# Optimization experiments

Measured on AMD Instinct MI355X. Metric: run time of the kernel, lower is better.

## Reference

```python
import jax, jax.numpy as jnp
import numpy as np

LN_EPS = 1e-6


def setup_inputs() -> dict:
    key = jax.random.key(0)
    ks = jax.random.split(key, 8)
    B, T, V, r, c, D = 1, 2048, 50257, 16, 16, 1024
    rc = r * c
    return {
        "input_ids": jax.random.randint(ks[0], (B, T), 0, V),
        "token_to_mu_w": jax.random.normal(ks[1], (rc, V), jnp.float32) * 0.02,  # nn.Linear(V, rc).weight
        "pos_embedding": jax.random.normal(ks[2], (1, T, r, c), jnp.float32) * 0.02,
        "w1": jax.random.normal(ks[3], (D, rc), jnp.float32) * 0.05,  # Linear(rc, D).weight
        "b1": jnp.zeros((D,), jnp.float32),
        "ln_w": jnp.ones((D,), jnp.float32),
        "ln_b": jnp.zeros((D,), jnp.float32),
        "w2": jax.random.normal(ks[4], (V, D), jnp.float32) * 0.02,  # Linear(D, V).weight
        "b2": jnp.zeros((V,), jnp.float32),
    }


def reference(input_ids, token_to_mu_w, pos_embedding, w1, b1, ln_w, ln_b, w2, b2):
    B, T = input_ids.shape
    r, c = pos_embedding.shape[2], pos_embedding.shape[3]
    # one_hot(input_ids) @ W^T is exactly a row-gather of W^T (single nonzero per row)
    MU = jnp.take(token_to_mu_w.T, input_ids, axis=0)          # [B, T, rc]
    MU = MU.reshape(B, T, r, c) + pos_embedding[:, :T]         # [B, T, r, c]
    # n_layers = 0: no transformer blocks; dropout is identity in eval
    x = MU.reshape(B, T, r * c)
    h = jax.nn.gelu(jnp.einsum('btk,dk->btd', x, w1) + b1, approximate=False)
    mean = jnp.mean(h, axis=-1, keepdims=True)
    var = jnp.mean(jnp.square(h - mean), axis=-1, keepdims=True)
    h = (h - mean) * jax.lax.rsqrt(var + LN_EPS) * ln_w + ln_b
    logits = jnp.einsum('btd,vd->btv', h, w2) + b2             # [B, T, V]
    return logits, MU
```

## Files before the change

### kernel.cpp

```cpp
#include <hip/hip_runtime.h>
#include <hip/hip_bf16.h>
#include <math.h>

#define T_LEN 2048
#define RC 256
#define DIM 1024
#define VOCAB 50257
#define NT 32
#define SLOT 8192

using short8  = __attribute__((ext_vector_type(8))) short;
using f32x4   = __attribute__((ext_vector_type(4))) float;

#define VMCNT(n) asm volatile("s_waitcnt vmcnt(" #n ")" ::: "memory")
#define SCHED_FENCE() __builtin_amdgcn_sched_barrier(0)

__device__ __forceinline__ unsigned short f2bf(float f) {
    unsigned int u = __float_as_uint(f);
    u += 0x7fffu + ((u >> 16) & 1u);
    return (unsigned short)(u >> 16);
}

__device__ __forceinline__ unsigned int cvt_pk_bf16(float a, float b) {
    unsigned int r;
    asm volatile("v_cvt_pk_bf16_f32 %0, %1, %2" : "=v"(r) : "v"(a), "v"(b));
    return r;
}

__device__ __forceinline__ void async_load16(void* lds, const void* g) {
    __builtin_amdgcn_global_load_lds(
        (const __attribute__((address_space(1))) void*)g,
        (__attribute__((address_space(3))) void*)lds,
        16, 0, 0);
}

__global__ __launch_bounds__(256) void mu_kernel(
    const int* __restrict__ ids, const float* __restrict__ tokw,
    const float* __restrict__ pos, float* __restrict__ mu) {
    int t = blockIdx.x, k = threadIdx.x;
    int id = ids[t];
    float v = tokw[(size_t)k * VOCAB + id] + pos[t * RC + k];
    mu[t * RC + k] = v;
}

__global__ __launch_bounds__(256) void gemm1_gelu_kernel(
    const float* __restrict__ mu, const float* __restrict__ w1,
    const float* __restrict__ b1, float* __restrict__ hpre) {
    __shared__ float xs[16][RC];
    const int tg = blockIdx.x, ng = blockIdx.y, tid = threadIdx.x;
    const int t0 = tg * 16;
    {
        const float4* src = (const float4*)(mu + (size_t)t0 * RC);
        float4* dst = (float4*)&xs[0][0];
        #pragma unroll
        for (int i = 0; i < 4; ++i) dst[tid + 256 * i] = src[tid + 256 * i];
    }
    __syncthreads();
    const int d = ng * 256 + tid;
    float acc[16];
    const float bias = b1[d];
    #pragma unroll
    for (int t = 0; t < 16; ++t) acc[t] = bias;
    const float4* w1r = (const float4*)(w1 + (size_t)d * RC);
    for (int k4 = 0; k4 < RC / 4; ++k4) {
        const float4 w = w1r[k4];
        #pragma unroll
        for (int t = 0; t < 16; ++t) {
            const float4 xv = *(const float4*)&xs[t][k4 * 4];
            acc[t] += w.x * xv.x + w.y * xv.y + w.z * xv.z + w.w * xv.w;
        }
    }
    #pragma unroll
    for (int t = 0; t < 16; ++t) {
        float x = acc[t];
        float g = 0.5f * x * (1.0f + erff(x * 0.70710678118654752f));
        hpre[(size_t)(t0 + t) * DIM + d] = g;
    }
}

__global__ __launch_bounds__(256) void ln_kernel(
    const float* __restrict__ hpre, const float* __restrict__ lnw,
    const float* __restrict__ lnb, unsigned short* __restrict__ h) {
    const int t = blockIdx.x, tid = threadIdx.x;
    const float4 v = ((const float4*)(hpre + (size_t)t * DIM))[tid];
    float s  = v.x + v.y + v.z + v.w;
    float ss = v.x * v.x + v.y * v.y + v.z * v.z + v.w * v.w;
    #pragma unroll
    for (int off = 32; off > 0; off >>= 1) {
        s  += __shfl_down(s, off, 64);
        ss += __shfl_down(ss, off, 64);
    }
    __shared__ float red[8];
    const int wid = tid >> 6, lane = tid & 63;
    if (lane == 0) { red[wid] = s; red[4 + wid] = ss; }
    __syncthreads();
    const float S  = red[0] + red[1] + red[2] + red[3];
    const float SS = red[4] + red[5] + red[6] + red[7];
    const float mean = S * (1.0f / DIM);
    const float var  = SS * (1.0f / DIM) - mean * mean;
    const float inv  = 1.0f / sqrtf(var + 1e-6f);
    const float4 wv = ((const float4*)lnw)[tid];
    const float4 bv = ((const float4*)lnb)[tid];
    ushort4 o;
    o.x = f2bf((v.x - mean) * inv * wv.x + bv.x);
    o.y = f2bf((v.y - mean) * inv * wv.y + bv.y);
    o.z = f2bf((v.z - mean) * inv * wv.z + bv.z);
    o.w = f2bf((v.w - mean) * inv * wv.w + bv.w);
    ((ushort4*)h)[(size_t)t * (DIM / 4) + tid] = o;
}

__global__ __launch_bounds__(256) void cvt_kernel(
    const float* __restrict__ src, unsigned int* __restrict__ dst, int n8) {
    int i = blockIdx.x * 256 + threadIdx.x;
    const int stride = gridDim.x * 256;
    for (; i < n8; i += stride) {
        const float4 a = ((const float4*)src)[2 * i];
        const float4 b = ((const float4*)src)[2 * i + 1];
        uint4 o;
        o.x = cvt_pk_bf16(a.x, a.y);
        o.y = cvt_pk_bf16(a.z, a.w);
        o.z = cvt_pk_bf16(b.x, b.y);
        o.w = cvt_pk_bf16(b.z, b.w);
        ((uint4*)dst)[i] = o;
    }
}

__device__ __forceinline__ void stage_A512(
    const unsigned short* __restrict__ A, unsigned short* dst,
    int m0, int kt, int tid, int gsrc) {
    #pragma unroll
    for (int p = 0; p < 2; ++p) {
        const int idx = p * 512 + tid;
        const int row = idx >> 2;
        async_load16(dst + (size_t)idx * 8,
                     A + (size_t)(m0 + row) * DIM + kt * 32 + gsrc * 8);
    }
}
__device__ __forceinline__ void stage_B512(
    const unsigned short* __restrict__ B, unsigned short* dst,
    int n0, int kt, int tid, int gsrc) {
    #pragma unroll
    for (int p = 0; p < 2; ++p) {
        const int idx = p * 512 + tid;
        int row = n0 + (idx >> 2); if (row > VOCAB - 1) row = VOCAB - 1;
        async_load16(dst + (size_t)idx * 8,
                     B + (size_t)row * DIM + kt * 32 + gsrc * 8);
    }
}

__global__ __launch_bounds__(512, 2) void gemm2_kernel(
    const unsigned short* __restrict__ A, const unsigned short* __restrict__ B,
    const float* __restrict__ b2, float* __restrict__ out) {
    __shared__ unsigned short As[3 * SLOT];
    __shared__ unsigned short Bs[3 * SLOT];

    const int tid  = threadIdx.x;
    const int cpx  = gridDim.x >> 3;
    const int wgid = (blockIdx.x & 7) * cpx + (blockIdx.x >> 3);
    const int m0   = (wgid & 7) << 8;
    const int n0   = (wgid >> 3) << 8;

    const int lane = tid & 63;
    const int lr   = lane & 15;
    const int lk   = lane >> 4;
    const int wid  = tid >> 6;
    const int wr   = wid >> 2;
    const int wc   = wid & 3;
    const int xr   = (lk ^ ((lr >> 1) & 3)) * 8;
    const int arow0 = wr * 128 + lr;
    const int brow0 = wc * 64 + lr;
    const int gsrc = (tid & 3) ^ ((tid >> 3) & 3);

    f32x4 acc[8][4];
    #pragma unroll
    for (int m = 0; m < 8; ++m)
        #pragma unroll
        for (int n = 0; n < 4; ++n) acc[m][n] = {0.f, 0.f, 0.f, 0.f};

    stage_A512(A, As, m0, 0, tid, gsrc);
    stage_B512(B, Bs, n0, 0, tid, gsrc);
    SCHED_FENCE();
    stage_A512(A, As + SLOT, m0, 1, tid, gsrc);
    stage_B512(B, Bs + SLOT, n0, 1, tid, gsrc);
    SCHED_FENCE();
    VMCNT(4);
    __builtin_amdgcn_s_barrier();

    int cur = 0, st2 = 2;
    #pragma unroll 1
    for (int t = 0; t < NT; ++t) {
        const unsigned short* As_t = As + cur * SLOT;
        const unsigned short* Bs_t = Bs + cur * SLOT;
        short8 af[4], af2[4], bf[4];

        #pragma unroll
        for (int m = 0; m < 4; ++m)
            af[m] = *(const short8*)(As_t + (arow0 + m * 16) * 32 + xr);
        #pragma unroll
        for (int n = 0; n < 4; ++n)
            bf[n] = *(const short8*)(Bs_t + (brow0 + n * 16) * 32 + xr);
        if (t + 2 < NT)
            stage_A512(A, As + st2 * SLOT, m0, t + 2, tid, gsrc);
        SCHED_FENCE();
        __builtin_amdgcn_s_barrier();
        __builtin_amdgcn_s_setprio(1);
        #pragma unroll
        for (int m = 0; m < 4; ++m)
            #pragma unroll
            for (int n = 0; n < 4; ++n)
                acc[m][n] = __builtin_amdgcn_mfma_f32_16x16x32_bf16(
                    af[m], bf[n], acc[m][n], 0, 0, 0);
        __builtin_amdgcn_s_setprio(0);
        SCHED_FENCE();
        __builtin_amdgcn_s_barrier();

        #pragma unroll
        for (int m = 0; m < 4; ++m)
            af2[m] = *(const short8*)(As_t + (arow0 + (m + 4) * 16) * 32 + xr);
        if (t + 2 < NT)
            stage_B512(B, Bs + st2 * SLOT, n0, t + 2, tid, gsrc);
        SCHED_FENCE();
        if (t < NT - 2) { VMCNT(4); } else { VMCNT(0); }
        __builtin_amdgcn_s_barrier();
        __builtin_amdgcn_s_setprio(1);
        #pragma unroll
        for (int m = 0; m < 4; ++m)
            #pragma unroll
            for (int n = 0; n < 4; ++n)
                acc[m + 4][n] = __builtin_amdgcn_mfma_f32_16x16x32_bf16(
                    af2[m], bf[n], acc[m + 4][n], 0, 0, 0);
        __builtin_amdgcn_s_setprio(0);
        SCHED_FENCE();
        __builtin_amdgcn_s_barrier();

        cur = (cur == 2) ? 0 : cur + 1;
        st2 = (st2 == 2) ? 0 : st2 + 1;
    }

    float bias[4]; int col[4]; bool ok[4];
    #pragma unroll
    for (int n = 0; n < 4; ++n) {
        col[n] = n0 + wc * 64 + n * 16 + lr;
        ok[n]  = col[n] < VOCAB;
        bias[n] = ok[n] ? b2[col[n]] : 0.f;
    }
    #pragma unroll
    for (int m = 0; m < 8; ++m) {
        const int row = m0 + wr * 128 + m * 16 + lk * 4;
        #pragma unroll
        for (int n = 0; n < 4; ++n) {
            if (ok[n]) {
                #pragma unroll
                for (int j = 0; j < 4; ++j)
                    out[(size_t)(row + j) * VOCAB + col[n]] = acc[m][n][j] + bias[n];
            }
        }
    }
}

extern "C" void kernel_launch(void* const* d_in, const int* in_sizes, int n_in,
                              void* d_out, int out_size, void* d_ws, size_t ws_size,
                              hipStream_t stream) {
    (void)in_sizes; (void)n_in; (void)out_size; (void)ws_size;
    const int*   ids  = (const int*)d_in[0];
    const float* tokw = (const float*)d_in[1];
    const float* pos  = (const float*)d_in[2];
    const float* w1   = (const float*)d_in[3];
    const float* b1   = (const float*)d_in[4];
    const float* lnw  = (const float*)d_in[5];
    const float* lnb  = (const float*)d_in[6];
    const float* w2   = (const float*)d_in[7];
    const float* b2   = (const float*)d_in[8];

    float* logits = (float*)d_out;
    float* mu_out = logits + (size_t)T_LEN * VOCAB;

    unsigned short* w2b = (unsigned short*)d_ws;
    unsigned short* hb  = (unsigned short*)((char*)d_ws + (size_t)VOCAB * DIM * 2);
    float* hpre = logits;

    mu_kernel<<<dim3(T_LEN), dim3(256), 0, stream>>>(ids, tokw, pos, mu_out);
    gemm1_gelu_kernel<<<dim3(T_LEN / 16, DIM / 256), dim3(256), 0, stream>>>(
        mu_out, w1, b1, hpre);
    ln_kernel<<<dim3(T_LEN), dim3(256), 0, stream>>>(hpre, lnw, lnb, hb);
    cvt_kernel<<<dim3(2048), dim3(256), 0, stream>>>(
        w2, (unsigned int*)w2b, (int)((size_t)VOCAB * DIM / 8));
    const int ntiles_n = (VOCAB + 255) / 256;
    gemm2_kernel<<<dim3(8 * ntiles_n), dim3(512), 0, stream>>>(hb, w2b, b2, logits);
}
```

Before: 464.2 us.

## Deepen gemm2 LDS pipeline to four stages with register-prefetched fragments

The output GEMM's shared-memory ring grows from three to four slots, so global loads are issued three K-tiles ahead instead of two. The loop is unrolled by two with ping-pong B-fragment registers. The next tile's A and B fragments are read from LDS before the second MFMA half of the current tile, and fine-grained lgkmcnt waits replace some of the barriers, cutting the barriers per tile from four to two. The aim is to hide LDS and global-load latency behind MFMA work, at the cost of more LDS and more live registers.

```diff
diff --git a/kernel.cpp b/kernel.cpp
--- a/kernel.cpp
+++ b/kernel.cpp
@@ -13,6 +13,7 @@
 using f32x4   = __attribute__((ext_vector_type(4))) float;
 
 #define VMCNT(n) asm volatile("s_waitcnt vmcnt(" #n ")" ::: "memory")
+#define LGKM(n)  asm volatile("s_waitcnt lgkmcnt(" #n ")" ::: "memory")
 #define SCHED_FENCE() __builtin_amdgcn_sched_barrier(0)
 
 __device__ __forceinline__ unsigned short f2bf(float f) {
@@ -148,11 +149,66 @@
     }
 }
 
+#define TILE_BODY(T, BF_USE, BF_LOAD)                                          \
+  {                                                                            \
+    const int t_  = (T);                                                       \
+    const int cur = t_ & 3;                                                    \
+    const int nxt = (t_ + 1) & 3;                                              \
+    const int st  = (t_ + 3) & 3;                                              \
+    const unsigned short* As_t = As + cur * SLOT;                              \
+                       \
+    _Pragma("unroll")                                                          \
+    for (int m = 0; m < 4; ++m)                                                \
+        af_o[m] = *(const short8*)(As_t + (arow0 + (m + 4) * 16) * 32 + xr);   \
+    if (t_ + 3 < NT)                                                           \
+        stage_A512(A, As + st * SLOT, m0, t_ + 3, tid, gsrc);                  \
+    SCHED_FENCE();                                                             \
+    LGKM(4);                           \
+    SCHED_FENCE();                                                             \
+    __builtin_amdgcn_s_setprio(1);                                             \
+    _Pragma("unroll")                                                          \
+    for (int m = 0; m < 4; ++m)                                                \
+        _Pragma("unroll")                                                      \
+        for (int n = 0; n < 4; ++n)                                            \
+            acc[m][n] = __builtin_amdgcn_mfma_f32_16x16x32_bf16(               \
+                af_e[m], BF_USE[n], acc[m][n], 0, 0, 0);                       \
+    __builtin_amdgcn_s_setprio(0);                                             \
+    SCHED_FENCE();                                                             \
+    if (t_ + 3 < NT) { VMCNT(6); } else { VMCNT(0); }                          \
+    __builtin_amdgcn_s_barrier();        \
+                        \
+    if (t_ + 1 < NT) {                                                         \
+        const unsigned short* As_n = As + nxt * SLOT;                          \
+        const unsigned short* Bs_n = Bs + nxt * SLOT;                          \
+        _Pragma("unroll")                                                      \
+        for (int m = 0; m < 4; ++m)                                            \
+            af_e[m] = *(const short8*)(As_n + (arow0 + m * 16) * 32 + xr);     \
+        _Pragma("unroll")                                                      \
+        for (int n = 0; n < 4; ++n)                                            \
+            BF_LOAD[n] = *(const short8*)(Bs_n + (brow0 + n * 16) * 32 + xr);  \
+    }                                                                          \
+    if (t_ + 3 < NT)                                                           \
+        stage_B512(B, Bs + st * SLOT, n0, t_ + 3, tid, gsrc);                  \
+    SCHED_FENCE();                                                             \
+    if (t_ + 1 < NT) { LGKM(8); } else { LGKM(0); }           \
+    SCHED_FENCE();                                                             \
+    __builtin_amdgcn_s_setprio(1);                                             \
+    _Pragma("unroll")                                                          \
+    for (int m = 0; m < 4; ++m)                                                \
+        _Pragma("unroll")                                                      \
+        for (int n = 0; n < 4; ++n)                                            \
+            acc[m + 4][n] = __builtin_amdgcn_mfma_f32_16x16x32_bf16(           \
+                af_o[m], BF_USE[n], acc[m + 4][n], 0, 0, 0);                   \
+    __builtin_amdgcn_s_setprio(0);                                             \
+    SCHED_FENCE();                                                             \
+    __builtin_amdgcn_s_barrier();     \
+  }
+
 __global__ __launch_bounds__(512, 2) void gemm2_kernel(
     const unsigned short* __restrict__ A, const unsigned short* __restrict__ B,
     const float* __restrict__ b2, float* __restrict__ out) {
-    __shared__ unsigned short As[3 * SLOT];
-    __shared__ unsigned short Bs[3 * SLOT];
+    __shared__ unsigned short As[4 * SLOT];
+    __shared__ unsigned short Bs[4 * SLOT];
 
     const int tid  = threadIdx.x;
     const int cpx  = gridDim.x >> 3;
@@ -183,58 +239,24 @@
     stage_A512(A, As + SLOT, m0, 1, tid, gsrc);
     stage_B512(B, Bs + SLOT, n0, 1, tid, gsrc);
     SCHED_FENCE();
-    VMCNT(4);
+    stage_A512(A, As + 2 * SLOT, m0, 2, tid, gsrc);
+    stage_B512(B, Bs + 2 * SLOT, n0, 2, tid, gsrc);
+    SCHED_FENCE();
+    VMCNT(8);
     __builtin_amdgcn_s_barrier();
 
-    int cur = 0, st2 = 2;
+    short8 af_e[4], af_o[4], bfA[4], bfB[4];
+    #pragma unroll
+    for (int m = 0; m < 4; ++m)
+        af_e[m] = *(const short8*)(As + (arow0 + m * 16) * 32 + xr);
+    #pragma unroll
+    for (int n = 0; n < 4; ++n)
+        bfA[n] = *(const short8*)(Bs + (brow0 + n * 16) * 32 + xr);
+
     #pragma unroll 1
-    for (int t = 0; t < NT; ++t) {
-        const unsigned short* As_t = As + cur * SLOT;
-        const unsigned short* Bs_t = Bs + cur * SLOT;
-        short8 af[4], af2[4], bf[4];
-
-        #pragma unroll
-        for (int m = 0; m < 4; ++m)
-            af[m] = *(const short8*)(As_t + (arow0 + m * 16) * 32 + xr);
-        #pragma unroll
-        for (int n = 0; n < 4; ++n)
-            bf[n] = *(const short8*)(Bs_t + (brow0 + n * 16) * 32 + xr);
-        if (t + 2 < NT)
-            stage_A512(A, As + st2 * SLOT, m0, t + 2, tid, gsrc);
-        SCHED_FENCE();
-        __builtin_amdgcn_s_barrier();
-        __builtin_amdgcn_s_setprio(1);
-        #pragma unroll
-        for (int m = 0; m < 4; ++m)
-            #pragma unroll
-            for (int n = 0; n < 4; ++n)
-                acc[m][n] = __builtin_amdgcn_mfma_f32_16x16x32_bf16(
-                    af[m], bf[n], acc[m][n], 0, 0, 0);
-        __builtin_amdgcn_s_setprio(0);
-        SCHED_FENCE();
-        __builtin_amdgcn_s_barrier();
-
-        #pragma unroll
-        for (int m = 0; m < 4; ++m)
-            af2[m] = *(const short8*)(As_t + (arow0 + (m + 4) * 16) * 32 + xr);
-        if (t + 2 < NT)
-            stage_B512(B, Bs + st2 * SLOT, n0, t + 2, tid, gsrc);
-        SCHED_FENCE();
-        if (t < NT - 2) { VMCNT(4); } else { VMCNT(0); }
-        __builtin_amdgcn_s_barrier();
-        __builtin_amdgcn_s_setprio(1);
-        #pragma unroll
-        for (int m = 0; m < 4; ++m)
-            #pragma unroll
-            for (int n = 0; n < 4; ++n)
-                acc[m + 4][n] = __builtin_amdgcn_mfma_f32_16x16x32_bf16(
-                    af2[m], bf[n], acc[m + 4][n], 0, 0, 0);
-        __builtin_amdgcn_s_setprio(0);
-        SCHED_FENCE();
-        __builtin_amdgcn_s_barrier();
-
-        cur = (cur == 2) ? 0 : cur + 1;
-        st2 = (st2 == 2) ? 0 : st2 + 1;
+    for (int tt = 0; tt < NT; tt += 2) {
+        TILE_BODY(tt,     bfA, bfB);
+        TILE_BODY(tt + 1, bfB, bfA);
     }
 
     float bias[4]; int col[4]; bool ok[4];
```

Result: no change. 461.0 us (-0.7%).

## Convert vocab GEMM to persistent kernel with atomic tile scheduler and cross-tile prefetch

Applied to the files above, without the earlier changes.

The output GEMM becomes a persistent kernel with a fixed grid of 512 workgroups. Each workgroup pulls 256x128 tiles from a global atomic counter, seeded by a new tiny kernel. The next tile's first K-stages are prefetched during the current tile's last iterations, hiding pipeline ramp-up, and the block is reduced to 256 threads with a narrower N tile. This trades larger per-tile reuse for better load balance on the tail, at the cost of an extra launch and atomic traffic. Barriers per K-step also drop from four to two.

```diff
diff --git a/kernel.cpp b/kernel.cpp
--- a/kernel.cpp
+++ b/kernel.cpp
@@ -6,13 +6,17 @@
 #define RC 256
 #define DIM 1024
 #define VOCAB 50257
-#define NT 32
-#define SLOT 8192
+#define NTILE_N 393
+#define NTILES (8 * NTILE_N)
+#define GRID_P 512
+#define ASLOT 8192
+#define BSLOT 4096
 
 using short8  = __attribute__((ext_vector_type(8))) short;
 using f32x4   = __attribute__((ext_vector_type(4))) float;
 
 #define VMCNT(n) asm volatile("s_waitcnt vmcnt(" #n ")" ::: "memory")
+#define LGKM0()  asm volatile("s_waitcnt lgkmcnt(0)" ::: "memory")
 #define SCHED_FENCE() __builtin_amdgcn_sched_barrier(0)
 
 __device__ __forceinline__ unsigned short f2bf(float f) {
@@ -33,6 +37,8 @@
         (__attribute__((address_space(3))) void*)lds,
         16, 0, 0);
 }
+
+__global__ void seed_kernel(unsigned int* ctr) { *ctr = GRID_P; }
 
 __global__ __launch_bounds__(256) void mu_kernel(
     const int* __restrict__ ids, const float* __restrict__ tokw,
@@ -125,47 +131,44 @@
     }
 }
 
-__device__ __forceinline__ void stage_A512(
+__device__ __forceinline__ void stage_A256(
     const unsigned short* __restrict__ A, unsigned short* dst,
     int m0, int kt, int tid, int gsrc) {
     #pragma unroll
-    for (int p = 0; p < 2; ++p) {
-        const int idx = p * 512 + tid;
+    for (int p = 0; p < 4; ++p) {
+        const int idx = p * 256 + tid;
         const int row = idx >> 2;
         async_load16(dst + (size_t)idx * 8,
                      A + (size_t)(m0 + row) * DIM + kt * 32 + gsrc * 8);
     }
 }
-__device__ __forceinline__ void stage_B512(
+__device__ __forceinline__ void stage_B256(
     const unsigned short* __restrict__ B, unsigned short* dst,
     int n0, int kt, int tid, int gsrc) {
     #pragma unroll
     for (int p = 0; p < 2; ++p) {
-        const int idx = p * 512 + tid;
+        const int idx = p * 256 + tid;
         int row = n0 + (idx >> 2); if (row > VOCAB - 1) row = VOCAB - 1;
         async_load16(dst + (size_t)idx * 8,
                      B + (size_t)row * DIM + kt * 32 + gsrc * 8);
     }
 }
 
-__global__ __launch_bounds__(512, 2) void gemm2_kernel(
+__global__ __launch_bounds__(256, 2) void gemm2_kernel(
     const unsigned short* __restrict__ A, const unsigned short* __restrict__ B,
-    const float* __restrict__ b2, float* __restrict__ out) {
-    __shared__ unsigned short As[3 * SLOT];
-    __shared__ unsigned short Bs[3 * SLOT];
+    const float* __restrict__ b2, float* __restrict__ out,
+    unsigned int* __restrict__ ctr) {
+    __shared__ unsigned short As[3 * ASLOT];
+    __shared__ unsigned short Bs[3 * BSLOT];
+    __shared__ int s_tau;
 
     const int tid  = threadIdx.x;
-    const int cpx  = gridDim.x >> 3;
-    const int wgid = (blockIdx.x & 7) * cpx + (blockIdx.x >> 3);
-    const int m0   = (wgid & 7) << 8;
-    const int n0   = (wgid >> 3) << 8;
-
     const int lane = tid & 63;
     const int lr   = lane & 15;
     const int lk   = lane >> 4;
     const int wid  = tid >> 6;
-    const int wr   = wid >> 2;
-    const int wc   = wid & 3;
+    const int wr   = wid >> 1;
+    const int wc   = wid & 1;
     const int xr   = (lk ^ ((lr >> 1) & 3)) * 8;
     const int arow0 = wr * 128 + lr;
     const int brow0 = wc * 64 + lr;
@@ -177,84 +180,109 @@
         #pragma unroll
         for (int n = 0; n < 4; ++n) acc[m][n] = {0.f, 0.f, 0.f, 0.f};
 
-    stage_A512(A, As, m0, 0, tid, gsrc);
-    stage_B512(B, Bs, n0, 0, tid, gsrc);
-    SCHED_FENCE();
-    stage_A512(A, As + SLOT, m0, 1, tid, gsrc);
-    stage_B512(B, Bs + SLOT, n0, 1, tid, gsrc);
-    SCHED_FENCE();
-    VMCNT(4);
+    int tau = blockIdx.x;
+    if (tid == 0) s_tau = (int)atomicAdd(ctr, 1u);
+
+    {
+        const int m0 = (tau & 7) << 8, n0 = (tau >> 3) << 7;
+        stage_A256(A, As, m0, 0, tid, gsrc);
+        stage_B256(B, Bs, n0, 0, tid, gsrc);
+        stage_A256(A, As + ASLOT, m0, 1, tid, gsrc);
+        stage_B256(B, Bs + BSLOT, n0, 1, tid, gsrc);
+    }
+    VMCNT(6);
+    LGKM0();
     __builtin_amdgcn_s_barrier();
 
-    int cur = 0, st2 = 2;
-    #pragma unroll 1
-    for (int t = 0; t < NT; ++t) {
-        const unsigned short* As_t = As + cur * SLOT;
-        const unsigned short* Bs_t = Bs + cur * SLOT;
-        short8 af[4], af2[4], bf[4];
-
-        #pragma unroll
-        for (int m = 0; m < 4; ++m)
-            af[m] = *(const short8*)(As_t + (arow0 + m * 16) * 32 + xr);
-        #pragma unroll
-        for (int n = 0; n < 4; ++n)
-            bf[n] = *(const short8*)(Bs_t + (brow0 + n * 16) * 32 + xr);
-        if (t + 2 < NT)
-            stage_A512(A, As + st2 * SLOT, m0, t + 2, tid, gsrc);
-        SCHED_FENCE();
-        __builtin_amdgcn_s_barrier();
-        __builtin_amdgcn_s_setprio(1);
-        #pragma unroll
-        for (int m = 0; m < 4; ++m)
+    int cur = 0, st = 2;
+    int tau_n = 0;
+
+    while (true) {
+        const int m0 = (tau & 7) << 8;
+        const int n0 = (tau >> 3) << 7;
+
+        #pragma unroll 1
+        for (int t = 0; t < 32; ++t) {
+            if (t == 0) tau_n = s_tau;
+            if (t == 16 && tid == 0)
+                s_tau = (int)atomicAdd(ctr, 1u);
+
+            const unsigned short* As_t = As + cur * ASLOT;
+            const unsigned short* Bs_t = Bs + cur * BSLOT;
+            bool st_ok; int sm0, sn0, sk;
+            if (t < 30) { st_ok = true; sm0 = m0; sn0 = n0; sk = t + 2; }
+            else {
+                st_ok = (tau_n < NTILES);
+                sm0 = (tau_n & 7) << 8; sn0 = (tau_n >> 3) << 7; sk = t - 30;
+            }
+
+            short8 af[4], bf[4], ag[4];
+            #pragma unroll
+            for (int m = 0; m < 4; ++m)
+                af[m] = *(const short8*)(As_t + (arow0 + m * 16) * 32 + xr);
             #pragma unroll
             for (int n = 0; n < 4; ++n)
-                acc[m][n] = __builtin_amdgcn_mfma_f32_16x16x32_bf16(
-                    af[m], bf[n], acc[m][n], 0, 0, 0);
-        __builtin_amdgcn_s_setprio(0);
-        SCHED_FENCE();
-        __builtin_amdgcn_s_barrier();
-
-        #pragma unroll
-        for (int m = 0; m < 4; ++m)
-            af2[m] = *(const short8*)(As_t + (arow0 + (m + 4) * 16) * 32 + xr);
-        if (t + 2 < NT)
-            stage_B512(B, Bs + st2 * SLOT, n0, t + 2, tid, gsrc);
-        SCHED_FENCE();
-        if (t < NT - 2) { VMCNT(4); } else { VMCNT(0); }
-        __builtin_amdgcn_s_barrier();
-        __builtin_amdgcn_s_setprio(1);
-        #pragma unroll
-        for (int m = 0; m < 4; ++m)
-            #pragma unroll
-            for (int n = 0; n < 4; ++n)
-                acc[m + 4][n] = __builtin_amdgcn_mfma_f32_16x16x32_bf16(
-                    af2[m], bf[n], acc[m + 4][n], 0, 0, 0);
-        __builtin_amdgcn_s_setprio(0);
-        SCHED_FENCE();
-        __builtin_amdgcn_s_barrier();
-
-        cur = (cur == 2) ? 0 : cur + 1;
-        st2 = (st2 == 2) ? 0 : st2 + 1;
-    }
-
-    float bias[4]; int col[4]; bool ok[4];
-    #pragma unroll
-    for (int n = 0; n < 4; ++n) {
-        col[n] = n0 + wc * 64 + n * 16 + lr;
-        ok[n]  = col[n] < VOCAB;
-        bias[n] = ok[n] ? b2[col[n]] : 0.f;
-    }
-    #pragma unroll
-    for (int m = 0; m < 8; ++m) {
-        const int row = m0 + wr * 128 + m * 16 + lk * 4;
-        #pragma unroll
-        for (int n = 0; n < 4; ++n) {
-            if (ok[n]) {
+                bf[n] = *(const short8*)(Bs_t + (brow0 + n * 16) * 32 + xr);
+            if (st_ok) stage_A256(A, As + st * ASLOT, sm0, sk, tid, gsrc);
+            LGKM0();
+            SCHED_FENCE();
+            __builtin_amdgcn_s_setprio(1);
+            #pragma unroll
+            for (int m = 0; m < 4; ++m)
                 #pragma unroll
-                for (int j = 0; j < 4; ++j)
-                    out[(size_t)(row + j) * VOCAB + col[n]] = acc[m][n][j] + bias[n];
+                for (int n = 0; n < 4; ++n)
+                    acc[m][n] = __builtin_amdgcn_mfma_f32_16x16x32_bf16(
+                        af[m], bf[n], acc[m][n], 0, 0, 0);
+            __builtin_amdgcn_s_setprio(0);
+            if (st_ok) { VMCNT(4); } else { VMCNT(0); }
+            __builtin_amdgcn_s_barrier();
+
+            #pragma unroll
+            for (int m = 0; m < 4; ++m)
+                ag[m] = *(const short8*)(As_t + (arow0 + (m + 4) * 16) * 32 + xr);
+            if (st_ok) stage_B256(B, Bs + st * BSLOT, sn0, sk, tid, gsrc);
+            LGKM0();
+            SCHED_FENCE();
+            __builtin_amdgcn_s_setprio(1);
+            #pragma unroll
+            for (int m = 0; m < 4; ++m)
+                #pragma unroll
+                for (int n = 0; n < 4; ++n)
+                    acc[m + 4][n] = __builtin_amdgcn_mfma_f32_16x16x32_bf16(
+                        ag[m], bf[n], acc[m + 4][n], 0, 0, 0);
+            __builtin_amdgcn_s_setprio(0);
+            __builtin_amdgcn_s_barrier();
+
+            cur = (cur == 2) ? 0 : cur + 1;
+            st  = (st  == 2) ? 0 : st  + 1;
+        }
+
+        {
+            float bias[4]; int col[4]; bool okn[4];
+            #pragma unroll
+            for (int n = 0; n < 4; ++n) {
+                col[n] = n0 + wc * 64 + n * 16 + lr;
+                okn[n] = col[n] < VOCAB;
+                bias[n] = okn[n] ? b2[col[n]] : 0.f;
+            }
+            #pragma unroll
+            for (int m = 0; m < 8; ++m) {
+                const int row = m0 + wr * 128 + m * 16 + lk * 4;
+                #pragma unroll
+                for (int n = 0; n < 4; ++n) {
+                    if (okn[n]) {
+                        #pragma unroll
+                        for (int j = 0; j < 4; ++j)
+                            out[(size_t)(row + j) * VOCAB + col[n]] =
+                                acc[m][n][j] + bias[n];
+                    }
+                    acc[m][n] = {0.f, 0.f, 0.f, 0.f};
+                }
             }
         }
+
+        if (tau_n >= NTILES) break;
+        tau = tau_n;
     }
 }
 
@@ -277,14 +305,16 @@
 
     unsigned short* w2b = (unsigned short*)d_ws;
     unsigned short* hb  = (unsigned short*)((char*)d_ws + (size_t)VOCAB * DIM * 2);
+    unsigned int*   ctr = (unsigned int*)((char*)d_ws + (size_t)VOCAB * DIM * 2
+                                          + (size_t)T_LEN * DIM * 2);
     float* hpre = logits;
 
+    seed_kernel<<<dim3(1), dim3(1), 0, stream>>>(ctr);
     mu_kernel<<<dim3(T_LEN), dim3(256), 0, stream>>>(ids, tokw, pos, mu_out);
     gemm1_gelu_kernel<<<dim3(T_LEN / 16, DIM / 256), dim3(256), 0, stream>>>(
         mu_out, w1, b1, hpre);
     ln_kernel<<<dim3(T_LEN), dim3(256), 0, stream>>>(hpre, lnw, lnb, hb);
     cvt_kernel<<<dim3(2048), dim3(256), 0, stream>>>(
         w2, (unsigned int*)w2b, (int)((size_t)VOCAB * DIM / 8));
-    const int ntiles_n = (VOCAB + 255) / 256;
-    gemm2_kernel<<<dim3(8 * ntiles_n), dim3(512), 0, stream>>>(hb, w2b, b2, logits);
-}
+    gemm2_kernel<<<dim3(GRID_P), dim3(256), 0, stream>>>(hb, w2b, b2, logits, ctr);
+}
```

After: 470.7 us (median of 2 runs). Within noise of the previous version (+1.4%).

## Restructure logits GEMM to BK=64 double-buffered half-tile pipeline

Applied to the files above, without the earlier changes.

The vocab-projection GEMM now uses a K-step of 64 instead of 32, with two LDS buffers in place of three. Each buffer is split into half-tiles whose async loads are issued between four MFMA sub-phases, and LDS uses an XOR swizzle over 8 chunks. This halves the number of main-loop iterations and barriers per K and interleaves global loads with compute at finer granularity. LDS use doubles, so occupancy drops to one workgroup per CU, and the hand-tuned vmcnt and barrier ordering must exactly match the staging sequence.

```diff
diff --git a/kernel.cpp b/kernel.cpp
--- a/kernel.cpp
+++ b/kernel.cpp
@@ -6,13 +6,15 @@
 #define RC 256
 #define DIM 1024
 #define VOCAB 50257
-#define NT 32
-#define SLOT 8192
+#define NT2 16
+#define SLOTW 16384
+#define HALFW 8192
 
 using short8  = __attribute__((ext_vector_type(8))) short;
 using f32x4   = __attribute__((ext_vector_type(4))) float;
 
 #define VMCNT(n) asm volatile("s_waitcnt vmcnt(" #n ")" ::: "memory")
+#define LGKM0()  asm volatile("s_waitcnt lgkmcnt(0)" ::: "memory")
 #define SCHED_FENCE() __builtin_amdgcn_sched_barrier(0)
 
 __device__ __forceinline__ unsigned short f2bf(float f) {
@@ -125,34 +127,37 @@
     }
 }
 
-__device__ __forceinline__ void stage_A512(
+__device__ __forceinline__ void stage_halfA(
     const unsigned short* __restrict__ A, unsigned short* dst,
-    int m0, int kt, int tid, int gsrc) {
+    int m0, int half, int kt, int tid) {
     #pragma unroll
     for (int p = 0; p < 2; ++p) {
         const int idx = p * 512 + tid;
-        const int row = idx >> 2;
+        const int r   = idx >> 3;
+        const int gl  = (idx & 7) ^ (r & 7);
         async_load16(dst + (size_t)idx * 8,
-                     A + (size_t)(m0 + row) * DIM + kt * 32 + gsrc * 8);
-    }
-}
-__device__ __forceinline__ void stage_B512(
+                     A + (size_t)(m0 + half * 128 + r) * DIM + kt * 64 + gl * 8);
+    }
+}
+__device__ __forceinline__ void stage_halfB(
     const unsigned short* __restrict__ B, unsigned short* dst,
-    int n0, int kt, int tid, int gsrc) {
+    int n0, int half, int kt, int tid) {
     #pragma unroll
     for (int p = 0; p < 2; ++p) {
         const int idx = p * 512 + tid;
-        int row = n0 + (idx >> 2); if (row > VOCAB - 1) row = VOCAB - 1;
+        const int r   = idx >> 3;
+        const int gl  = (idx & 7) ^ (r & 7);
+        int row = n0 + half * 128 + r; if (row > VOCAB - 1) row = VOCAB - 1;
         async_load16(dst + (size_t)idx * 8,
-                     B + (size_t)row * DIM + kt * 32 + gsrc * 8);
-    }
-}
-
-__global__ __launch_bounds__(512, 2) void gemm2_kernel(
+                     B + (size_t)row * DIM + kt * 64 + gl * 8);
+    }
+}
+
+__global__ __launch_bounds__(512, 1) void gemm2_kernel(
     const unsigned short* __restrict__ A, const unsigned short* __restrict__ B,
     const float* __restrict__ b2, float* __restrict__ out) {
-    __shared__ unsigned short As[3 * SLOT];
-    __shared__ unsigned short Bs[3 * SLOT];
+    __shared__ unsigned short As[2 * SLOTW];
+    __shared__ unsigned short Bs[2 * SLOTW];
 
     const int tid  = threadIdx.x;
     const int cpx  = gridDim.x >> 3;
@@ -166,10 +171,7 @@
     const int wid  = tid >> 6;
     const int wr   = wid >> 2;
     const int wc   = wid & 3;
-    const int xr   = (lk ^ ((lr >> 1) & 3)) * 8;
-    const int arow0 = wr * 128 + lr;
-    const int brow0 = wc * 64 + lr;
-    const int gsrc = (tid & 3) ^ ((tid >> 3) & 3);
+    const int sx   = lr & 7;
 
     f32x4 acc[8][4];
     #pragma unroll
@@ -177,64 +179,109 @@
         #pragma unroll
         for (int n = 0; n < 4; ++n) acc[m][n] = {0.f, 0.f, 0.f, 0.f};
 
-    stage_A512(A, As, m0, 0, tid, gsrc);
-    stage_B512(B, Bs, n0, 0, tid, gsrc);
-    SCHED_FENCE();
-    stage_A512(A, As + SLOT, m0, 1, tid, gsrc);
-    stage_B512(B, Bs + SLOT, n0, 1, tid, gsrc);
-    SCHED_FENCE();
-    VMCNT(4);
+    stage_halfB(B, Bs,                 n0, 0, 0, tid);
+    stage_halfB(B, Bs + HALFW,         n0, 1, 0, tid);
+    stage_halfA(A, As,                 m0, 0, 0, tid);
+    stage_halfA(A, As + HALFW,         m0, 1, 0, tid);
+    stage_halfB(B, Bs + SLOTW,         n0, 0, 1, tid);
+    stage_halfB(B, Bs + SLOTW + HALFW, n0, 1, 1, tid);
+    stage_halfA(A, As + SLOTW,         m0, 0, 1, tid);
+    VMCNT(6);
     __builtin_amdgcn_s_barrier();
 
-    int cur = 0, st2 = 2;
+    short8 af[8], bfr[8];
+
     #pragma unroll 1
-    for (int t = 0; t < NT; ++t) {
-        const unsigned short* As_t = As + cur * SLOT;
-        const unsigned short* Bs_t = Bs + cur * SLOT;
-        short8 af[4], af2[4], bf[4];
-
-        #pragma unroll
-        for (int m = 0; m < 4; ++m)
-            af[m] = *(const short8*)(As_t + (arow0 + m * 16) * 32 + xr);
-        #pragma unroll
-        for (int n = 0; n < 4; ++n)
-            bf[n] = *(const short8*)(Bs_t + (brow0 + n * 16) * 32 + xr);
-        if (t + 2 < NT)
-            stage_A512(A, As + st2 * SLOT, m0, t + 2, tid, gsrc);
+    for (int k = 0; k < NT2; ++k) {
+        const unsigned short* As_t = As + (k & 1) * SLOTW;
+        const unsigned short* Bs_t = Bs + (k & 1) * SLOTW;
+        unsigned short* As_n  = As + ((k + 1) & 1) * SLOTW;
+        unsigned short* As_n2 = As + (k & 1) * SLOTW;
+        unsigned short* Bs_n2 = Bs + (k & 1) * SLOTW;
+
+        #pragma unroll
+        for (int mi = 0; mi < 4; ++mi) {
+            const int R = wr * 128 + mi * 16 + lr;
+            #pragma unroll
+            for (int kk = 0; kk < 2; ++kk)
+                af[mi * 2 + kk] =
+                    *(const short8*)(As_t + R * 64 + (((kk * 4 + lk) ^ sx) << 3));
+        }
+        #pragma unroll
+        for (int ni = 0; ni < 4; ++ni) {
+            const int R = wc * 64 + ni * 16 + lr;
+            #pragma unroll
+            for (int kk = 0; kk < 2; ++kk)
+                bfr[ni * 2 + kk] =
+                    *(const short8*)(Bs_t + R * 64 + (((kk * 4 + lk) ^ sx) << 3));
+        }
+        if (k + 1 < NT2) stage_halfA(A, As_n + HALFW, m0, 1, k + 1, tid);
+        __builtin_amdgcn_s_barrier();
+        LGKM0();
         SCHED_FENCE();
-        __builtin_amdgcn_s_barrier();
         __builtin_amdgcn_s_setprio(1);
         #pragma unroll
-        for (int m = 0; m < 4; ++m)
-            #pragma unroll
-            for (int n = 0; n < 4; ++n)
-                acc[m][n] = __builtin_amdgcn_mfma_f32_16x16x32_bf16(
-                    af[m], bf[n], acc[m][n], 0, 0, 0);
+        for (int mi = 0; mi < 4; ++mi)
+            #pragma unroll
+            for (int ni = 0; ni < 2; ++ni)
+                #pragma unroll
+                for (int kk = 0; kk < 2; ++kk)
+                    acc[mi][ni] = __builtin_amdgcn_mfma_f32_16x16x32_bf16(
+                        af[mi * 2 + kk], bfr[ni * 2 + kk], acc[mi][ni], 0, 0, 0);
         __builtin_amdgcn_s_setprio(0);
+        __builtin_amdgcn_s_barrier();
+
+        if (k + 2 < NT2) stage_halfB(B, Bs_n2, n0, 0, k + 2, tid);
+        __builtin_amdgcn_s_setprio(1);
+        #pragma unroll
+        for (int mi = 0; mi < 4; ++mi)
+            #pragma unroll
+            for (int ni = 2; ni < 4; ++ni)
+                #pragma unroll
+                for (int kk = 0; kk < 2; ++kk)
+                    acc[mi][ni] = __builtin_amdgcn_mfma_f32_16x16x32_bf16(
+                        af[mi * 2 + kk], bfr[ni * 2 + kk], acc[mi][ni], 0, 0, 0);
+        __builtin_amdgcn_s_setprio(0);
+        __builtin_amdgcn_s_barrier();
+
+        #pragma unroll
+        for (int mi = 0; mi < 4; ++mi) {
+            const int R = wr * 128 + (mi + 4) * 16 + lr;
+            #pragma unroll
+            for (int kk = 0; kk < 2; ++kk)
+                af[mi * 2 + kk] =
+                    *(const short8*)(As_t + R * 64 + (((kk * 4 + lk) ^ sx) << 3));
+        }
+        if (k + 2 < NT2) stage_halfB(B, Bs_n2 + HALFW, n0, 1, k + 2, tid);
+        __builtin_amdgcn_s_barrier();
+        LGKM0();
         SCHED_FENCE();
-        __builtin_amdgcn_s_barrier();
-
-        #pragma unroll
-        for (int m = 0; m < 4; ++m)
-            af2[m] = *(const short8*)(As_t + (arow0 + (m + 4) * 16) * 32 + xr);
-        if (t + 2 < NT)
-            stage_B512(B, Bs + st2 * SLOT, n0, t + 2, tid, gsrc);
-        SCHED_FENCE();
-        if (t < NT - 2) { VMCNT(4); } else { VMCNT(0); }
-        __builtin_amdgcn_s_barrier();
         __builtin_amdgcn_s_setprio(1);
         #pragma unroll
-        for (int m = 0; m < 4; ++m)
-            #pragma unroll
-            for (int n = 0; n < 4; ++n)
-                acc[m + 4][n] = __builtin_amdgcn_mfma_f32_16x16x32_bf16(
-                    af2[m], bf[n], acc[m + 4][n], 0, 0, 0);
+        for (int mi = 0; mi < 4; ++mi)
+            #pragma unroll
+            for (int ni = 0; ni < 2; ++ni)
+                #pragma unroll
+                for (int kk = 0; kk < 2; ++kk)
+                    acc[mi + 4][ni] = __builtin_amdgcn_mfma_f32_16x16x32_bf16(
+                        af[mi * 2 + kk], bfr[ni * 2 + kk], acc[mi + 4][ni], 0, 0, 0);
         __builtin_amdgcn_s_setprio(0);
-        SCHED_FENCE();
-        __builtin_amdgcn_s_barrier();
-
-        cur = (cur == 2) ? 0 : cur + 1;
-        st2 = (st2 == 2) ? 0 : st2 + 1;
+        __builtin_amdgcn_s_barrier();
+
+        if (k + 2 < NT2) stage_halfA(A, As_n2, m0, 0, k + 2, tid);
+        __builtin_amdgcn_s_setprio(1);
+        #pragma unroll
+        for (int mi = 0; mi < 4; ++mi)
+            #pragma unroll
+            for (int ni = 2; ni < 4; ++ni)
+                #pragma unroll
+                for (int kk = 0; kk < 2; ++kk)
+                    acc[mi + 4][ni] = __builtin_amdgcn_mfma_f32_16x16x32_bf16(
+                        af[mi * 2 + kk], bfr[ni * 2 + kk], acc[mi + 4][ni], 0, 0, 0);
+        __builtin_amdgcn_s_setprio(0);
+        if (k < NT2 - 2)       { VMCNT(6); }
+        else if (k == NT2 - 2) { VMCNT(0); }
+        __builtin_amdgcn_s_barrier();
     }
 
     float bias[4]; int col[4]; bool ok[4];
```

Measured after the change: 482.4 us. 1.04x slower.
